# Optimization experiments

Measured on AMD Instinct MI355X. Metric: run time of the kernel, lower is better.

Reference implementation:

```python
import jax, jax.numpy as jnp
import numpy as np

B, S, H, D = 2, 2048, 32, 128
DM = H * D  # 4096
SCALE = D ** -0.5


def setup_inputs() -> dict:
    key = jax.random.key(0)
    ks = jax.random.split(key, 7)
    std = DM ** -0.5
    return {
        "q": jax.random.normal(ks[0], (B, S, DM), dtype=jnp.float32),
        "k": jax.random.normal(ks[1], (B, S, DM), dtype=jnp.float32),
        "v": jax.random.normal(ks[2], (B, S, DM), dtype=jnp.float32),
        # torch nn.Linear weights are [out_features, in_features]
        "Wq": jax.random.normal(ks[3], (DM, DM), dtype=jnp.float32) * std,
        "Wk": jax.random.normal(ks[4], (DM, DM), dtype=jnp.float32) * std,
        "Wv": jax.random.normal(ks[5], (DM, DM), dtype=jnp.float32) * std,
        "Wo": jax.random.normal(ks[6], (DM, DM), dtype=jnp.float32) * std,
    }


def reference(q, k, v, Wq, Wk, Wv, Wo):
    # Linear: y = x @ W^T (no bias, qkv_bias=False)
    qp = q @ Wq.T  # [B,S,DM]
    kp = k @ Wk.T
    vp = v @ Wv.T
    # [B,S,DM] -> [B,H,S,D]
    qh = qp.reshape(B, S, H, D).transpose(0, 2, 1, 3)
    kh = kp.reshape(B, S, H, D).transpose(0, 2, 1, 3)
    vh = vp.reshape(B, S, H, D).transpose(0, 2, 1, 3)
    # scaled dot-product attention (no mask; attn_mask default None)
    scores = jnp.einsum("bhqd,bhkd->bhqk", qh, kh) * SCALE  # [B,H,S,S]
    probs = jax.nn.softmax(scores, axis=-1)
    ctx = jnp.einsum("bhqk,bhkd->bhqd", probs, vh)  # [B,H,S,D]
    ctx = ctx.transpose(0, 2, 1, 3).reshape(B, S, DM)
    return ctx @ Wo.T  # [B,S,DM]
```

## Files before the change

### kernel.cpp

```cpp
#include <hip/hip_runtime.h>
#include <hip/hip_bf16.h>
#include <stdint.h>


using u16 = unsigned short;
using u32 = unsigned int;

typedef __attribute__((ext_vector_type(8))) short bf16x8;
typedef __attribute__((ext_vector_type(8))) u16 u16x8;
typedef __attribute__((ext_vector_type(4))) u16 u16x4;
typedef __attribute__((ext_vector_type(4))) float f32x4;

#define MFMA_BF16(A, B, C) __builtin_amdgcn_mfma_f32_16x16x32_bf16((A), (B), (C), 0, 0, 0)

static constexpr int kS = 2048, kDM = 4096, kD = 128;
static constexpr size_t kMat = (size_t)4096 * 4096;
static constexpr float kScaleLog2e = 0.08838834764831845f * 1.44269504088896340736f;

static __device__ __forceinline__ void gload_lds16(const u16* g, u16* l) {
  __builtin_amdgcn_global_load_lds((const __attribute__((address_space(1))) void*)g,
                                   (__attribute__((address_space(3))) void*)l, 16, 0, 0);
}

static __device__ __forceinline__ u16 f2bf(float f) {
  u32 u = __float_as_uint(f);
  u32 r = u + 0x7FFFu + ((u >> 16) & 1u);
  return (u16)(r >> 16);
}

static __device__ __forceinline__ float bf2f(u16 x) {
  return __uint_as_float((u32)x << 16);
}

static __device__ __forceinline__ u16 nbf(float f) {
  union { __hip_bfloat16 h; u16 u; } cv;
  cv.h = __float2bfloat16(f);
  return cv.u;
}

static __device__ __forceinline__ u16x8 cvt8(float4 a, float4 b) {
  u16x8 r;
  r[0] = f2bf(a.x); r[1] = f2bf(a.y); r[2] = f2bf(a.z); r[3] = f2bf(a.w);
  r[4] = f2bf(b.x); r[5] = f2bf(b.y); r[6] = f2bf(b.z); r[7] = f2bf(b.w);
  return r;
}

__global__ __launch_bounds__(256) void cvt_kernel(
    const float* __restrict__ s0, const float* __restrict__ s1,
    const float* __restrict__ s2, const float* __restrict__ s3,
    const float* __restrict__ s4, const float* __restrict__ s5,
    const float* __restrict__ s6, u16* __restrict__ dst) {
  const int y = blockIdx.y;
  const float* s = (y == 0) ? s0 : (y == 1) ? s1 : (y == 2) ? s2 : (y == 3) ? s3
                  : (y == 4) ? s4 : (y == 5) ? s5 : s6;
  u16* d = dst + (size_t)y * kMat;
  const size_t nchunk = kMat / 8;
  const size_t step = (size_t)gridDim.x * 256;
  for (size_t c = (size_t)blockIdx.x * 256 + threadIdx.x; c < nchunk; c += step) {
    const float* p = s + c * 8;
    float4 a = *(const float4*)p;
    float4 b = *(const float4*)(p + 4);
    *(u16x8*)(d + c * 8) = cvt8(a, b);
  }
}

template <bool TRANS, bool OUT_F32>
static __device__ __forceinline__ void gemm256(const u16* __restrict__ X,
                                               const u16* __restrict__ W,
                                               void* __restrict__ Yv,
                                               u16* __restrict__ lds,
                                               int m0, int n0) {
  constexpr int NT = kDM / 64;
  const int tid = threadIdx.x;
  const int lane = tid & 63;
  const int w = tid >> 6;
  const int fr = lane & 15;
  const int fq = lane >> 4;
  const int wr = w >> 2;
  const int wc = w & 3;

  const int srow = tid >> 3;
  const int scol = ((tid & 7) ^ (srow & 7)) * 8;
  const u16* Xrow = X + (size_t)(m0 + srow) * kDM + scol;
  const u16* Wrow = W + (size_t)(n0 + srow) * kDM + scol;
  const int w512 = w * 512;

  const int rBb = wc * 64 + fr;
  const int rAb = wr * 128 + fr;
  const int swz = fr & 7;

  f32x4 acc[8][4] = {};

#define STAGE2(ROWP, qrow, k0, ldq)                                        \
  do {                                                                     \
    gload_lds16((ROWP) + (size_t)(qrow) * kDM + (k0), &lds[(ldq) + w512]); \
    gload_lds16((ROWP) + (size_t)((qrow) + 64) * kDM + (k0),               \
                &lds[(ldq) + 4096 + w512]);                                \
  } while (0)

#define RD_B(BOFF, nf, ks) \
  (*(const bf16x8*)&lds[(BOFF) + (rBb + (nf) * 16) * 64 + ((((ks) * 4 + fq) ^ swz) * 8)])
#define RD_A(AOFF, mi, ks) \
  (*(const bf16x8*)&lds[(AOFF) + (rAb + (mi) * 16) * 64 + ((((ks) * 4 + fq) ^ swz) * 8)])

#define CLUSTER(mia)                                                            \
  do {                                                                          \
    __builtin_amdgcn_s_setprio(1);                                              \
    _Pragma("unroll") for (int mj = 0; mj < 2; ++mj)                            \
    _Pragma("unroll") for (int nf = 0; nf < 4; ++nf)                            \
    _Pragma("unroll") for (int ks = 0; ks < 2; ++ks)                            \
      acc[(mia) + mj][nf] =                                                     \
          TRANS ? MFMA_BF16(bfr[nf][ks], af[mj][ks], acc[(mia) + mj][nf])       \
                : MFMA_BF16(af[mj][ks], bfr[nf][ks], acc[(mia) + mj][nf]);      \
    __builtin_amdgcn_s_setprio(0);                                              \
  } while (0)

#define KTILE(DC, t)                                                           \
  {                                                                            \
    constexpr int Boff = (DC) * 32768;                                         \
    constexpr int Aoff = Boff + 16384;                                         \
    bf16x8 bfr[4][2], af[2][2];                                                \
                            \
    _Pragma("unroll") for (int nf = 0; nf < 4; ++nf)                           \
    _Pragma("unroll") for (int ks = 0; ks < 2; ++ks)                           \
      bfr[nf][ks] = RD_B(Boff, nf, ks);                                        \
    _Pragma("unroll") for (int mj = 0; mj < 2; ++mj)                           \
    _Pragma("unroll") for (int ks = 0; ks < 2; ++ks)                           \
      af[mj][ks] = RD_A(Aoff, mj, ks);                                         \
    if ((t) + 1 < NT)                                                          \
      STAGE2(Xrow, 128, ((t) + 1) * 64, ((DC) ^ 1) * 32768 + 24576);           \
    __builtin_amdgcn_s_barrier();                                              \
    CLUSTER(0);                                                                \
    __builtin_amdgcn_s_barrier();                                              \
                                      \
    _Pragma("unroll") for (int mj = 0; mj < 2; ++mj)                           \
    _Pragma("unroll") for (int ks = 0; ks < 2; ++ks)                           \
      af[mj][ks] = RD_A(Aoff, 2 + mj, ks);                                     \
    if ((t) + 2 < NT) STAGE2(Wrow, 0, ((t) + 2) * 64, Boff + 0);               \
    __builtin_amdgcn_s_barrier();                                              \
    CLUSTER(2);                                                                \
    __builtin_amdgcn_s_barrier();                                              \
                                      \
    _Pragma("unroll") for (int mj = 0; mj < 2; ++mj)                           \
    _Pragma("unroll") for (int ks = 0; ks < 2; ++ks)                           \
      af[mj][ks] = RD_A(Aoff, 4 + mj, ks);                                     \
    if ((t) + 2 < NT) STAGE2(Wrow, 128, ((t) + 2) * 64, Boff + 8192);          \
    __builtin_amdgcn_s_barrier();                                              \
    CLUSTER(4);                                                                \
    __builtin_amdgcn_s_barrier();                                              \
                            \
    _Pragma("unroll") for (int mj = 0; mj < 2; ++mj)                           \
    _Pragma("unroll") for (int ks = 0; ks < 2; ++ks)                           \
      af[mj][ks] = RD_A(Aoff, 6 + mj, ks);                                     \
    if ((t) + 2 < NT) STAGE2(Xrow, 0, ((t) + 2) * 64, Boff + 16384);           \
    __builtin_amdgcn_s_barrier();                                              \
    CLUSTER(6);                                                                \
    if ((t) + 2 < NT)                                                          \
      asm volatile("s_waitcnt vmcnt(6)" ::: "memory");                         \
    else                                                                       \
      asm volatile("s_waitcnt vmcnt(0)" ::: "memory");                         \
    __builtin_amdgcn_s_barrier();                                              \
  }

  STAGE2(Wrow, 0, 0, 0);
  STAGE2(Wrow, 128, 0, 8192);
  STAGE2(Xrow, 0, 0, 16384);
  STAGE2(Xrow, 128, 0, 24576);
  STAGE2(Wrow, 0, 64, 32768);
  STAGE2(Wrow, 128, 64, 32768 + 8192);
  STAGE2(Xrow, 0, 64, 32768 + 16384);
  asm volatile("s_waitcnt vmcnt(6)" ::: "memory");
  __builtin_amdgcn_s_barrier();

  for (int tt = 0; tt < NT; tt += 2) {
    KTILE(0, tt);
    KTILE(1, tt + 1);
  }
#undef KTILE
#undef CLUSTER
#undef RD_A
#undef RD_B
#undef STAGE2

#pragma unroll
  for (int mi = 0; mi < 8; ++mi)
#pragma unroll
    for (int nf = 0; nf < 4; ++nf) {
      int row, col;
      if constexpr (TRANS) {
        row = n0 + wc * 64 + nf * 16 + fq * 4;
        col = m0 + wr * 128 + mi * 16 + fr;
      } else {
        row = m0 + wr * 128 + mi * 16 + fq * 4;
        col = n0 + wc * 64 + nf * 16 + fr;
      }
      if constexpr (OUT_F32) {
        float* yp = (float*)Yv + (size_t)row * kDM + col;
#pragma unroll
        for (int i = 0; i < 4; ++i) yp[(size_t)i * kDM] = acc[mi][nf][i];
      } else {
        u16* yp = (u16*)Yv + (size_t)row * kDM + col;
#pragma unroll
        for (int i = 0; i < 4; ++i) yp[(size_t)i * kDM] = f2bf(acc[mi][nf][i]);
      }
    }
}

static __device__ __forceinline__ int xcd_swz(int id, int cpx) {
  return (id & 7) * cpx + (id >> 3);
}

__global__ __launch_bounds__(512, 2) void proj_qk256_kernel(const u16* __restrict__ wsb,
                                                            u16* __restrict__ qp,
                                                            u16* __restrict__ kp) {
  __shared__ u16 lds[65536];
  const int z = blockIdx.z;
  const int s = xcd_swz(blockIdx.y * 16 + blockIdx.x, 32);
  const int m0 = (s >> 4) * 256, n0 = (s & 15) * 256;
  gemm256<false, false>(wsb + (size_t)z * kMat, wsb + (size_t)(3 + z) * kMat,
                        z ? kp : qp, lds, m0, n0);
}

__global__ __launch_bounds__(512, 2) void proj_vT256_kernel(const u16* __restrict__ wsb,
                                                            u16* __restrict__ vpT) {
  __shared__ u16 lds[65536];
  const int s = xcd_swz(blockIdx.y * 16 + blockIdx.x, 32);
  gemm256<true, false>(wsb + 2 * kMat, wsb + 5 * kMat, vpT, lds,
                       (s >> 4) * 256, (s & 15) * 256);
}

__global__ __launch_bounds__(512, 2) void out_proj256_kernel(const u16* __restrict__ ctx,
                                                             const u16* __restrict__ Wob,
                                                             float* __restrict__ out) {
  __shared__ u16 lds[65536];
  const int s = xcd_swz(blockIdx.y * 16 + blockIdx.x, 32);
  gemm256<false, true>(ctx, Wob, out, lds, (s >> 4) * 256, (s & 15) * 256);
}

template <bool A_BF16, bool TRANS, bool OUT_F32>
static __device__ __forceinline__ void gemm_conv(const void* Xv, const float* Wf,
                                                 void* Yv, u16* __restrict__ Als,
                                                 u16* __restrict__ Bls) {
  constexpr int KD = 4096;
  const int tid = threadIdx.x;
  const int lane = tid & 63;
  const int w = tid >> 6;
  const int fr = lane & 15;
  const int fq = lane >> 4;
  const int m0 = blockIdx.y * 128;
  const int n0 = blockIdx.x * 128;

  const int r0 = tid >> 2, cc0 = (tid & 3) * 8;
  const int r1 = r0 + 64;
  const int sr = lane >> 2, sc = (lane & 3) * 8;
  const int u0 = w * 2, u1 = w * 2 + 1;

  const u16* Xb = (const u16*)Xv;
  const float* Xf = (const float*)Xv;

  const int wm = (w >> 1) * 64;
  const int wn = (w & 1) * 64;

  f32x4 acc[4][4] = {};

  for (int kt = 0; kt < KD / 32; ++kt) {
    const int ko = kt * 32;
    if constexpr (A_BF16) {
      gload_lds16(Xb + (size_t)(m0 + u0 * 16 + sr) * KD + ko + sc, &Als[u0 * 512]);
      gload_lds16(Xb + (size_t)(m0 + u1 * 16 + sr) * KD + ko + sc, &Als[u1 * 512]);
    } else {
      const float* p0 = Xf + (size_t)(m0 + r0) * KD + ko + cc0;
      const float* p1 = Xf + (size_t)(m0 + r1) * KD + ko + cc0;
      float4 a0 = *(const float4*)(p0);
      float4 a1 = *(const float4*)(p0 + 4);
      float4 a2 = *(const float4*)(p1);
      float4 a3 = *(const float4*)(p1 + 4);
      *(u16x8*)&Als[r0 * 32 + cc0] = cvt8(a0, a1);
      *(u16x8*)&Als[r1 * 32 + cc0] = cvt8(a2, a3);
    }
    {
      const float* p0 = Wf + (size_t)(n0 + r0) * KD + ko + cc0;
      const float* p1 = Wf + (size_t)(n0 + r1) * KD + ko + cc0;
      float4 b0 = *(const float4*)(p0);
      float4 b1 = *(const float4*)(p0 + 4);
      float4 b2 = *(const float4*)(p1);
      float4 b3 = *(const float4*)(p1 + 4);
      *(u16x8*)&Bls[r0 * 32 + cc0] = cvt8(b0, b1);
      *(u16x8*)&Bls[r1 * 32 + cc0] = cvt8(b2, b3);
    }
    __syncthreads();

    bf16x8 af[4], bfv[4];
#pragma unroll
    for (int i = 0; i < 4; ++i)
      af[i] = *(const bf16x8*)&Als[(wm + i * 16 + fr) * 32 + fq * 8];
#pragma unroll
    for (int i = 0; i < 4; ++i)
      bfv[i] = *(const bf16x8*)&Bls[(wn + i * 16 + fr) * 32 + fq * 8];
#pragma unroll
    for (int a = 0; a < 4; ++a)
#pragma unroll
      for (int bb = 0; bb < 4; ++bb) {
        if constexpr (TRANS)
          acc[a][bb] = MFMA_BF16(bfv[a], af[bb], acc[a][bb]);
        else
          acc[a][bb] = MFMA_BF16(af[a], bfv[bb], acc[a][bb]);
      }
    __syncthreads();
  }

#pragma unroll
  for (int a = 0; a < 4; ++a)
#pragma unroll
    for (int bb = 0; bb < 4; ++bb) {
      const int row = TRANS ? (n0 + wn + a * 16 + fq * 4) : (m0 + wm + a * 16 + fq * 4);
      const int col = TRANS ? (m0 + wm + bb * 16 + fr) : (n0 + wn + bb * 16 + fr);
      if constexpr (OUT_F32) {
        float* yp = (float*)Yv + (size_t)row * kDM + col;
#pragma unroll
        for (int i = 0; i < 4; ++i) yp[(size_t)i * kDM] = acc[a][bb][i];
      } else {
        u16* yp = (u16*)Yv + (size_t)row * kDM + col;
#pragma unroll
        for (int i = 0; i < 4; ++i) yp[(size_t)i * kDM] = f2bf(acc[a][bb][i]);
      }
    }
}

__global__ __launch_bounds__(256) void proj_qk_conv_kernel(
    const float* __restrict__ q, const float* __restrict__ k,
    const float* __restrict__ Wq, const float* __restrict__ Wk,
    u16* __restrict__ qp, u16* __restrict__ kp) {
  __shared__ u16 Als[128 * 32];
  __shared__ u16 Bls[128 * 32];
  const int z = blockIdx.z;
  gemm_conv<false, false, false>(z ? k : q, z ? Wk : Wq, z ? kp : qp, Als, Bls);
}

__global__ __launch_bounds__(256) void proj_vT_conv_kernel(
    const float* __restrict__ v, const float* __restrict__ Wv, u16* __restrict__ vpT) {
  __shared__ u16 Als[128 * 32];
  __shared__ u16 Bls[128 * 32];
  gemm_conv<false, true, false>(v, Wv, vpT, Als, Bls);
}

__global__ __launch_bounds__(256) void out_proj_conv_kernel(const u16* __restrict__ ctx,
                                                            const float* __restrict__ Wo,
                                                            float* __restrict__ out) {
  __shared__ u16 Als[128 * 32];
  __shared__ u16 Bls[128 * 32];
  gemm_conv<true, false, true>(ctx, Wo, out, Als, Bls);
}

__global__ __launch_bounds__(512) void attn_kernel(const u16* __restrict__ qp,
                                                   const u16* __restrict__ kp,
                                                   const u16* __restrict__ vpT,
                                                   u16* __restrict__ ctx) {
  constexpr int KB = 64;
  constexpr int NT = kS / KB;
  constexpr int PST = 72;
  constexpr float THR = 11.5f;

  __shared__ u16 Kls[KB * 128];
  __shared__ u16 Vt[kD * KB];
  __shared__ u16 Pls[8][2 * 16 * PST];

  const int tid = threadIdx.x, lane = tid & 63, w = tid >> 6;
  const int fr = lane & 15, fq = lane >> 4;

  const int wg = blockIdx.y * 8 + blockIdx.x;
  const int o = (wg & 7) * 64 + (wg >> 3);
  const int bh = o >> 3;
  const int b = bh >> 5, h = bh & 31;
  const int q0 = (o & 7) * 256;

  const u16* qbase = qp + ((size_t)b * kS) * kDM + h * kD;
  const u16* kbase = kp + ((size_t)b * kS) * kDM + h * kD;
  const u16* vtbase = vpT + (size_t)(h * kD) * kDM + b * kS;

  bf16x8 qf[2][4];
#pragma unroll
  for (int rb = 0; rb < 2; ++rb)
#pragma unroll
    for (int kc = 0; kc < 4; ++kc) {
      const u16x8 raw = *(const u16x8*)(qbase +
          (size_t)(q0 + w * 32 + rb * 16 + fr) * kDM + kc * 32 + fq * 8);
      bf16x8 s;
#pragma unroll
      for (int j = 0; j < 8; ++j) s[j] = (short)f2bf(bf2f(raw[j]) * kScaleLog2e);
      qf[rb][kc] = s;
    }

  f32x4 oacc[2][9] = {};
  float mrun[2] = {-1e30f, -1e30f};

  bf16x8 ones;
#pragma unroll
  for (int j = 0; j < 8; ++j) ones[j] = (short)0x3F80;

  const int krl = lane >> 4, kdp = lane & 15;
  const int vdl = lane >> 3, vc = lane & 7;
  const int rk0 = (w * 2 + 0) * 4 + krl;
  const int rk1 = (w * 2 + 1) * 4 + krl;
  const int dv0 = (w * 2 + 0) * 8 + vdl;
  const int dv1 = (w * 2 + 1) * 8 + vdl;
  const u16* kg0 = kbase + (size_t)rk0 * kDM + kdp * 8;
  const u16* kg1 = kbase + (size_t)rk1 * kDM + kdp * 8;
  const u16* vg0 = vtbase + (size_t)dv0 * kDM + vc * 8;
  const u16* vg1 = vtbase + (size_t)dv1 * kDM + vc * 8;
  u16* kl0 = &Kls[rk0 * 128 + ((kdp ^ (rk0 & 7)) * 8)];
  u16* kl1 = &Kls[rk1 * 128 + ((kdp ^ (rk1 & 7)) * 8)];
  u16* vl0 = &Vt[dv0 * KB + ((vc ^ (dv0 & 7)) * 8)];
  u16* vl1 = &Vt[dv1 * KB + ((vc ^ (dv1 & 7)) * 8)];

  u16x8 kr0v, kr1v, vr0v, vr1v;
  kr0v = *(const u16x8*)kg0;
  kr1v = *(const u16x8*)kg1;
  vr0v = *(const u16x8*)vg0;
  vr1v = *(const u16x8*)vg1;
  *(u16x8*)kl0 = kr0v; *(u16x8*)kl1 = kr1v;
  *(u16x8*)vl0 = vr0v; *(u16x8*)vl1 = vr1v;
  __syncthreads();

  for (int kt = 0; kt < NT; ++kt) {
    if (kt + 1 < NT) {
      const size_t ko = (size_t)(kt + 1) * KB;
      kr0v = *(const u16x8*)(kg0 + ko * kDM);
      kr1v = *(const u16x8*)(kg1 + ko * kDM);
      vr0v = *(const u16x8*)(vg0 + ko);
      vr1v = *(const u16x8*)(vg1 + ko);
    }

    f32x4 sacc[2][4] = {};
#pragma unroll
    for (int cb = 0; cb < 4; ++cb) {
      const int n = cb * 16 + fr;
      bf16x8 kf[4];
#pragma unroll
      for (int kc = 0; kc < 4; ++kc) {
        const int d0 = kc * 4 + fq;
        kf[kc] = *(const bf16x8*)&Kls[n * 128 + (d0 ^ (n & 7)) * 8];
      }
      __builtin_amdgcn_s_setprio(1);
#pragma unroll
      for (int rb = 0; rb < 2; ++rb)
#pragma unroll
        for (int kc = 0; kc < 4; ++kc)
          sacc[rb][cb] = MFMA_BF16(kf[kc], qf[rb][kc], sacc[rb][cb]);
      __builtin_amdgcn_s_setprio(0);
    }

#pragma unroll
    for (int rb = 0; rb < 2; ++rb) {
      float m = sacc[rb][0][0];
#pragma unroll
      for (int cb = 0; cb < 4; ++cb)
#pragma unroll
        for (int i = 0; i < 4; ++i) m = fmaxf(m, sacc[rb][cb][i]);
      m = fmaxf(m, __shfl_xor(m, 16));
      m = fmaxf(m, __shfl_xor(m, 32));

      if (__any(m - mrun[rb] > THR)) {
        const float mnew = fmaxf(mrun[rb], m);
        const float sclS = exp2f(mrun[rb] - mnew);
        mrun[rb] = mnew;
        float scl[4];
#pragma unroll
        for (int i = 0; i < 4; ++i) scl[i] = __shfl(sclS, fq * 4 + i);
#pragma unroll
        for (int db = 0; db < 9; ++db)
#pragma unroll
          for (int i = 0; i < 4; ++i) oacc[rb][db][i] *= scl[i];
      }

#pragma unroll
      for (int cb = 0; cb < 4; ++cb) {
        u16x4 pk;
#pragma unroll
        for (int i = 0; i < 4; ++i)
          pk[i] = nbf(exp2f(sacc[rb][cb][i] - mrun[rb]));
        *(u16x4*)&Pls[w][rb * (16 * PST) + fr * PST + cb * 16 + fq * 4] = pk;
      }
    }

    asm volatile("s_waitcnt lgkmcnt(0)" ::: "memory");

    bf16x8 pf[2][2];
#pragma unroll
    for (int rb = 0; rb < 2; ++rb)
#pragma unroll
      for (int kb = 0; kb < 2; ++kb)
        pf[rb][kb] = *(const bf16x8*)&Pls[w][rb * (16 * PST) + fr * PST + kb * 32 + fq * 8];
#pragma unroll
    for (int db = 0; db < 8; ++db) {
      const int d = db * 16 + fr;
      bf16x8 vf0 = *(const bf16x8*)&Vt[d * KB + ((fq ^ (d & 7)) << 3)];
      bf16x8 vf1 = *(const bf16x8*)&Vt[d * KB + (((4 + fq) ^ (d & 7)) << 3)];
      __builtin_amdgcn_s_setprio(1);
#pragma unroll
      for (int rb = 0; rb < 2; ++rb) {
        oacc[rb][db] = MFMA_BF16(pf[rb][0], vf0, oacc[rb][db]);
        oacc[rb][db] = MFMA_BF16(pf[rb][1], vf1, oacc[rb][db]);
      }
      __builtin_amdgcn_s_setprio(0);
    }
    __builtin_amdgcn_s_setprio(1);
#pragma unroll
    for (int rb = 0; rb < 2; ++rb) {
      oacc[rb][8] = MFMA_BF16(pf[rb][0], ones, oacc[rb][8]);
      oacc[rb][8] = MFMA_BF16(pf[rb][1], ones, oacc[rb][8]);
    }
    __builtin_amdgcn_s_setprio(0);

    __syncthreads();
    if (kt + 1 < NT) {
      *(u16x8*)kl0 = kr0v; *(u16x8*)kl1 = kr1v;
      *(u16x8*)vl0 = vr0v; *(u16x8*)vl1 = vr1v;
    }
    __syncthreads();
  }

  u16* cbase = ctx + ((size_t)b * kS) * kDM + h * kD;
#pragma unroll
  for (int rb = 0; rb < 2; ++rb) {
    float inv[4];
#pragma unroll
    for (int i = 0; i < 4; ++i) inv[i] = 1.0f / oacc[rb][8][i];
#pragma unroll
    for (int db = 0; db < 8; ++db)
#pragma unroll
      for (int i = 0; i < 4; ++i) {
        const int row = q0 + w * 32 + rb * 16 + fq * 4 + i;
        const int col = db * 16 + fr;
        cbase[(size_t)row * kDM + col] = nbf(oacc[rb][db][i] * inv[i]);
      }
  }
}

extern "C" void kernel_launch(void* const* d_in, const int* in_sizes, int n_in,
                              void* d_out, int out_size, void* d_ws, size_t ws_size,
                              hipStream_t stream) {
  const float* q = (const float*)d_in[0];
  const float* k = (const float*)d_in[1];
  const float* v = (const float*)d_in[2];
  const float* Wq = (const float*)d_in[3];
  const float* Wk = (const float*)d_in[4];
  const float* Wv = (const float*)d_in[5];
  const float* Wo = (const float*)d_in[6];
  float* out = (float*)d_out;

  const size_t needFast = 11 * kMat * sizeof(u16);

  if (ws_size >= needFast) {
    u16* wsb = (u16*)d_ws;
    u16* qp = wsb + 7 * kMat;
    u16* kp = wsb + 8 * kMat;
    u16* vpT = wsb + 9 * kMat;
    u16* ctx = wsb + 10 * kMat;

    cvt_kernel<<<dim3(1024, 7), 256, 0, stream>>>(q, k, v, Wq, Wk, Wv, Wo, wsb);
    proj_qk256_kernel<<<dim3(16, 16, 2), 512, 0, stream>>>(wsb, qp, kp);
    proj_vT256_kernel<<<dim3(16, 16), 512, 0, stream>>>(wsb, vpT);
    attn_kernel<<<dim3(8, 64), 512, 0, stream>>>(qp, kp, vpT, ctx);
    out_proj256_kernel<<<dim3(16, 16), 512, 0, stream>>>(ctx, wsb + 6 * kMat, out);
  } else {
    u16* qp = (u16*)d_ws;
    u16* kp = qp + kMat;
    u16* vpT = kp + kMat;
    u16* ctx = vpT + kMat;

    proj_qk_conv_kernel<<<dim3(32, 32, 2), 256, 0, stream>>>(q, k, Wq, Wk, qp, kp);
    proj_vT_conv_kernel<<<dim3(32, 32), 256, 0, stream>>>(v, Wv, vpT);
    attn_kernel<<<dim3(8, 64), 512, 0, stream>>>(qp, kp, vpT, ctx);
    out_proj_conv_kernel<<<dim3(32, 32, 1), 256, 0, stream>>>(ctx, Wo, out);
  }
}
```

Before: 745.2 us.

## Double-buffer LDS fragment registers to prefetch next k-tile during MFMA clusters

Result: slower. 1.316 ms (+76.6%).

```diff
diff --git a/kernel.cpp b/kernel.cpp
--- a/kernel.cpp
+++ b/kernel.cpp
@@ -90,6 +90,8 @@
   const int swz = fr & 7;
 
   f32x4 acc[8][4] = {};
+  bf16x8 bfrA[4][2], bfrB[4][2];
+  bf16x8 afA[2][2], afB[2][2];
 
 #define STAGE2(ROWP, qrow, k0, ldq)                                        \
   do {                                                                     \
@@ -103,62 +105,64 @@
 #define RD_A(AOFF, mi, ks) \
   (*(const bf16x8*)&lds[(AOFF) + (rAb + (mi) * 16) * 64 + ((((ks) * 4 + fq) ^ swz) * 8)])
 
-#define CLUSTER(mia)                                                            \
+#define CLUSTER(mia, BARR, AARR)                                                \
   do {                                                                          \
     __builtin_amdgcn_s_setprio(1);                                              \
     _Pragma("unroll") for (int mj = 0; mj < 2; ++mj)                            \
     _Pragma("unroll") for (int nf = 0; nf < 4; ++nf)                            \
     _Pragma("unroll") for (int ks = 0; ks < 2; ++ks)                            \
       acc[(mia) + mj][nf] =                                                     \
-          TRANS ? MFMA_BF16(bfr[nf][ks], af[mj][ks], acc[(mia) + mj][nf])       \
-                : MFMA_BF16(af[mj][ks], bfr[nf][ks], acc[(mia) + mj][nf]);      \
+          TRANS ? MFMA_BF16(BARR[nf][ks], AARR[mj][ks], acc[(mia) + mj][nf])    \
+                : MFMA_BF16(AARR[mj][ks], BARR[nf][ks], acc[(mia) + mj][nf]);   \
     __builtin_amdgcn_s_setprio(0);                                              \
   } while (0)
 
-#define KTILE(DC, t)                                                           \
+#define KTILE(DC, t, BC, BN)                                                   \
   {                                                                            \
     constexpr int Boff = (DC) * 32768;                                         \
     constexpr int Aoff = Boff + 16384;                                         \
-    bf16x8 bfr[4][2], af[2][2];                                                \
-                            \
-    _Pragma("unroll") for (int nf = 0; nf < 4; ++nf)                           \
-    _Pragma("unroll") for (int ks = 0; ks < 2; ++ks)                           \
-      bfr[nf][ks] = RD_B(Boff, nf, ks);                                        \
+    constexpr int BoffN = ((DC) ^ 1) * 32768;                                  \
+    constexpr int AoffN = BoffN + 16384;                                       \
+                          \
     _Pragma("unroll") for (int mj = 0; mj < 2; ++mj)                           \
     _Pragma("unroll") for (int ks = 0; ks < 2; ++ks)                           \
-      af[mj][ks] = RD_A(Aoff, mj, ks);                                         \
-    if ((t) + 1 < NT)                                                          \
-      STAGE2(Xrow, 128, ((t) + 1) * 64, ((DC) ^ 1) * 32768 + 24576);           \
-    __builtin_amdgcn_s_barrier();                                              \
-    CLUSTER(0);                                                                \
-    __builtin_amdgcn_s_barrier();                                              \
-                                      \
+      afB[mj][ks] = RD_A(Aoff, 2 + mj, ks);                                    \
+    if ((t) + 1 < NT) STAGE2(Xrow, 128, ((t) + 1) * 64, BoffN + 24576);        \
+    __builtin_amdgcn_s_barrier();                                              \
+    CLUSTER(0, BC, afA);                                                       \
+    __builtin_amdgcn_s_barrier();                                              \
+                          \
     _Pragma("unroll") for (int mj = 0; mj < 2; ++mj)                           \
     _Pragma("unroll") for (int ks = 0; ks < 2; ++ks)                           \
-      af[mj][ks] = RD_A(Aoff, 2 + mj, ks);                                     \
+      afA[mj][ks] = RD_A(Aoff, 4 + mj, ks);                                    \
     if ((t) + 2 < NT) STAGE2(Wrow, 0, ((t) + 2) * 64, Boff + 0);               \
     __builtin_amdgcn_s_barrier();                                              \
-    CLUSTER(2);                                                                \
-    __builtin_amdgcn_s_barrier();                                              \
-                                      \
+    CLUSTER(2, BC, afB);                                                       \
+    __builtin_amdgcn_s_barrier();                                              \
+                          \
     _Pragma("unroll") for (int mj = 0; mj < 2; ++mj)                           \
     _Pragma("unroll") for (int ks = 0; ks < 2; ++ks)                           \
-      af[mj][ks] = RD_A(Aoff, 4 + mj, ks);                                     \
+      afB[mj][ks] = RD_A(Aoff, 6 + mj, ks);                                    \
     if ((t) + 2 < NT) STAGE2(Wrow, 128, ((t) + 2) * 64, Boff + 8192);          \
     __builtin_amdgcn_s_barrier();                                              \
-    CLUSTER(4);                                                                \
-    __builtin_amdgcn_s_barrier();                                              \
-                            \
-    _Pragma("unroll") for (int mj = 0; mj < 2; ++mj)                           \
-    _Pragma("unroll") for (int ks = 0; ks < 2; ++ks)                           \
-      af[mj][ks] = RD_A(Aoff, 6 + mj, ks);                                     \
-    if ((t) + 2 < NT) STAGE2(Xrow, 0, ((t) + 2) * 64, Boff + 16384);           \
-    __builtin_amdgcn_s_barrier();                                              \
-    CLUSTER(6);                                                                \
+    CLUSTER(4, BC, afA);                                                       \
+    __builtin_amdgcn_s_barrier();                                              \
+                                                              \
     if ((t) + 2 < NT)                                                          \
-      asm volatile("s_waitcnt vmcnt(6)" ::: "memory");                         \
+      asm volatile("s_waitcnt vmcnt(4)" ::: "memory");                         \
     else                                                                       \
       asm volatile("s_waitcnt vmcnt(0)" ::: "memory");                         \
+    if ((t) + 1 < NT) {                                                        \
+      _Pragma("unroll") for (int nf = 0; nf < 4; ++nf)                         \
+      _Pragma("unroll") for (int ks = 0; ks < 2; ++ks)                         \
+        BN[nf][ks] = RD_B(BoffN, nf, ks);                                      \
+      _Pragma("unroll") for (int mj = 0; mj < 2; ++mj)                         \
+      _Pragma("unroll") for (int ks = 0; ks < 2; ++ks)                         \
+        afA[mj][ks] = RD_A(AoffN, mj, ks);                                     \
+    }                                                                          \
+    if ((t) + 2 < NT) STAGE2(Xrow, 0, ((t) + 2) * 64, Boff + 16384);           \
+    __builtin_amdgcn_s_barrier();                                              \
+    CLUSTER(6, BC, afB);                                                       \
     __builtin_amdgcn_s_barrier();                                              \
   }
 
@@ -171,10 +175,18 @@
   STAGE2(Xrow, 0, 64, 32768 + 16384);
   asm volatile("s_waitcnt vmcnt(6)" ::: "memory");
   __builtin_amdgcn_s_barrier();
+#pragma unroll
+  for (int nf = 0; nf < 4; ++nf)
+#pragma unroll
+    for (int ks = 0; ks < 2; ++ks) bfrA[nf][ks] = RD_B(0, nf, ks);
+#pragma unroll
+  for (int mj = 0; mj < 2; ++mj)
+#pragma unroll
+    for (int ks = 0; ks < 2; ++ks) afA[mj][ks] = RD_A(16384, mj, ks);
 
   for (int tt = 0; tt < NT; tt += 2) {
-    KTILE(0, tt);
-    KTILE(1, tt + 1);
+    KTILE(0, tt, bfrA, bfrB);
+    KTILE(1, tt + 1, bfrB, bfrA);
   }
 #undef KTILE
 #undef CLUSTER
```
